# Kernel tuning notes

Measured on AMD Instinct MI355X. Metric: run time of the kernel, lower is better.

## Reference

```python
import jax, jax.numpy as jnp
import numpy as np

ANGLE_BINS = 16
RADIUS_BINS = 8


def _bilinear_cart(img, ys, xs):
    # img [B,C,H,W]; ys/xs: sample grid [A,R] in pixel coords, zero outside image
    h, w = img.shape[2], img.shape[3]
    y0 = jnp.floor(ys)
    x0 = jnp.floor(xs)
    wy = (ys - y0).astype(img.dtype)
    wx = (xs - x0).astype(img.dtype)
    y0i = jnp.clip(y0, 0, h - 1).astype(jnp.int32)
    y1i = jnp.clip(y0 + 1, 0, h - 1).astype(jnp.int32)
    x0i = jnp.clip(x0, 0, w - 1).astype(jnp.int32)
    x1i = jnp.clip(x0 + 1, 0, w - 1).astype(jnp.int32)
    v00 = img[:, :, y0i, x0i]
    v01 = img[:, :, y0i, x1i]
    v10 = img[:, :, y1i, x0i]
    v11 = img[:, :, y1i, x1i]
    out = (v00 * (1 - wy) * (1 - wx) + v01 * (1 - wy) * wx
           + v10 * wy * (1 - wx) + v11 * wy * wx)
    valid = ((ys >= 0) & (ys <= h - 1) & (xs >= 0) & (xs <= w - 1)).astype(img.dtype)
    return out * valid


def cartesian_to_polar(x):
    # [B,C,H,W] -> [B,C,ANGLE_BINS,RADIUS_BINS] via bilinear sampling on a polar grid
    b, c, h, w = x.shape
    cy = (h - 1) / 2.0
    cx = (w - 1) / 2.0
    max_r = min(h, w) / 2.0
    theta = 2.0 * jnp.pi * jnp.arange(ANGLE_BINS, dtype=jnp.float32) / ANGLE_BINS
    r = (jnp.arange(RADIUS_BINS, dtype=jnp.float32) + 0.5) / RADIUS_BINS * max_r
    ys = cy + r[None, :] * jnp.sin(theta)[:, None]  # [A,R]
    xs = cx + r[None, :] * jnp.cos(theta)[:, None]  # [A,R]
    return _bilinear_cart(x, ys, xs)


def polar_to_cartesian(pf, h, w):
    # [B,C,A,R] -> [B,C,H,W]: inverse remap with angular wrap, radial clamp,
    # zero outside the max radius disc
    b, c, A, R = pf.shape
    cy = (h - 1) / 2.0
    cx = (w - 1) / 2.0
    max_r = min(h, w) / 2.0
    yy, xx = jnp.meshgrid(jnp.arange(h, dtype=jnp.float32),
                          jnp.arange(w, dtype=jnp.float32), indexing='ij')
    dy = yy - cy
    dx = xx - cx
    rr = jnp.sqrt(dy * dy + dx * dx)
    th = jnp.mod(jnp.arctan2(dy, dx), 2.0 * jnp.pi)
    a = th / (2.0 * jnp.pi) * A
    ri = rr / max_r * R - 0.5
    a0 = jnp.floor(a)
    wa = (a - a0).astype(pf.dtype)
    a0i = jnp.mod(a0.astype(jnp.int32), A)
    a1i = jnp.mod(a0i + 1, A)
    r0 = jnp.floor(ri)
    wr = (ri - r0).astype(pf.dtype)
    r0i = jnp.clip(r0, 0, R - 1).astype(jnp.int32)
    r1i = jnp.clip(r0 + 1, 0, R - 1).astype(jnp.int32)
    v00 = pf[:, :, a0i, r0i]
    v01 = pf[:, :, a0i, r1i]
    v10 = pf[:, :, a1i, r0i]
    v11 = pf[:, :, a1i, r1i]
    out = (v00 * (1 - wa) * (1 - wr) + v01 * (1 - wa) * wr
           + v10 * wa * (1 - wr) + v11 * wa * wr)
    valid = (rr <= max_r).astype(pf.dtype)
    return out * valid


def setup_inputs() -> dict:
    key = jax.random.key(0)
    ks = jax.random.split(key, 4)
    B, C, H, W = 16, 256, 128, 128
    x = jax.random.normal(ks[0], (B, C, H, W), dtype=jnp.float32)
    # grouped 3x3 conv: groups=4 -> kernel [C_out=C, C_in/groups=C//4, 3, 3]
    w_polar = jax.random.normal(ks[1], (C, C // 4, 3, 3), dtype=jnp.float32) * 0.05
    b_polar = jnp.zeros((C,), jnp.float32)
    w_attn1 = jax.random.normal(ks[2], (C // 4, C), dtype=jnp.float32) * 0.05
    b_attn1 = jnp.zeros((C // 4,), jnp.float32)
    w_attn2 = jax.random.normal(ks[3], (1, C // 4), dtype=jnp.float32) * 0.05
    b_attn2 = jnp.zeros((1,), jnp.float32)
    return {"x": x, "w_polar": w_polar, "b_polar": b_polar,
            "w_attn1": w_attn1, "b_attn1": b_attn1,
            "w_attn2": w_attn2, "b_attn2": b_attn2}


def reference(x, w_polar, b_polar, w_attn1, b_attn1, w_attn2, b_attn2):
    b, c, h, w = x.shape
    pf = cartesian_to_polar(x)  # [B,C,16,8]
    pp = jax.lax.conv_general_dilated(
        pf, w_polar, window_strides=(1, 1), padding=((1, 1), (1, 1)),
        dimension_numbers=('NCHW', 'OIHW', 'NCHW'), feature_group_count=4)
    pp = pp + b_polar[None, :, None, None]
    pc = polar_to_cartesian(pp, h, w)  # [B,C,H,W]
    h1 = jax.nn.relu(jnp.einsum('bchw,oc->bohw', pc, w_attn1)
                     + b_attn1[None, :, None, None])
    att = jax.nn.sigmoid(jnp.einsum('bchw,oc->bohw', h1, w_attn2)
                         + b_attn2[None, :, None, None])  # [B,1,H,W]
    return x * att
```

## Files before the change

kernel.cpp:

```cpp
#include <hip/hip_runtime.h>
#include <math.h>

#define TWO_PI 6.28318530717958647692f

typedef float f4 __attribute__((ext_vector_type(4)));

__global__ __launch_bounds__(256) void k1_cart2polar(const float* __restrict__ x,
                                                     float* __restrict__ pf) {
    __shared__ float w00s[128], w01s[128], w10s[128], w11s[128];
    __shared__ int   o00s[128], o01s[128], o10s[128], o11s[128];
    int tid = threadIdx.x;
    if (tid < 128) {
        int a = tid >> 3, r = tid & 7;
        float theta = (TWO_PI * (float)a) / 16.0f;
        float rad   = ((float)r + 0.5f) / 8.0f * 64.0f;
        float ys = 63.5f + rad * sinf(theta);
        float xs = 63.5f + rad * cosf(theta);
        float y0 = floorf(ys), x0 = floorf(xs);
        float wy = ys - y0,    wx = xs - x0;
        int y0i = min(max((int)y0, 0), 127);
        int y1i = min(max((int)y0 + 1, 0), 127);
        int x0i = min(max((int)x0, 0), 127);
        int x1i = min(max((int)x0 + 1, 0), 127);
        float valid = (ys >= 0.0f && ys <= 127.0f && xs >= 0.0f && xs <= 127.0f) ? 1.0f : 0.0f;
        w00s[tid] = valid * (1.0f - wy) * (1.0f - wx);
        w01s[tid] = valid * (1.0f - wy) * wx;
        w10s[tid] = valid * wy * (1.0f - wx);
        w11s[tid] = valid * wy * wx;
        o00s[tid] = y0i * 128 + x0i;
        o01s[tid] = y0i * 128 + x1i;
        o10s[tid] = y1i * 128 + x0i;
        o11s[tid] = y1i * 128 + x1i;
    }
    __syncthreads();
    int t = blockIdx.x * 256 + tid;
    int bin = t & 127;
    int img = t >> 7;
    const float* ib = x + ((size_t)img << 14);
    float v = ib[o00s[bin]] * w00s[bin]
            + ib[o01s[bin]] * w01s[bin]
            + ib[o10s[bin]] * w10s[bin]
            + ib[o11s[bin]] * w11s[bin];
    pf[t] = v;
}

__global__ __launch_bounds__(128) void k2_conv(const float* __restrict__ pf,
                                               const float* __restrict__ w_polar,
                                               const float* __restrict__ b_polar,
                                               float* __restrict__ pp_t) {
    __shared__ __align__(16) float pfs[32 * 180];
    __shared__ __align__(16) float wls[32 * 72];
    int bid = blockIdx.x;
    int b  = bid >> 5;
    int g  = (bid >> 3) & 3;
    int ot = bid & 7;
    int tid = threadIdx.x;
    int a = tid >> 3, r = tid & 7;
    int oc0 = g * 64 + ot * 8;

    for (int i = tid; i < 32 * 180; i += 128) pfs[i] = 0.0f;
    __syncthreads();

    float acc[8];
    #pragma unroll
    for (int j = 0; j < 8; ++j) acc[j] = 0.0f;
    const float* src = pf + ((size_t)(b * 256 + g * 64) << 7);

    for (int pass = 0; pass < 2; ++pass) {
        for (int i = tid; i < 4096; i += 128) {
            int icl = i >> 7, bin = i & 127;
            pfs[icl * 180 + ((bin >> 3) + 1) * 10 + (bin & 7) + 1]
                = src[pass * 4096 + i];
        }
        for (int i = tid; i < 2304; i += 128) {
            int icl = i / 72, rem = i - icl * 72;
            int tap = rem >> 3, j = rem & 7;
            wls[i] = w_polar[(size_t)(oc0 + j) * 576 + (pass * 32 + icl) * 9 + tap];
        }
        __syncthreads();

        const float* pbase = pfs + a * 10 + r;
        for (int ic = 0; ic < 32; ++ic) {
            float v[9];
            const float* base = pbase + ic * 180;
            #pragma unroll
            for (int dh = 0; dh < 3; ++dh)
                #pragma unroll
                for (int dw = 0; dw < 3; ++dw)
                    v[dh * 3 + dw] = base[dh * 10 + dw];
            const f4* wrow = (const f4*)(wls + ic * 72);
            #pragma unroll
            for (int tap = 0; tap < 9; ++tap) {
                f4 wlo = wrow[tap * 2];
                f4 whi = wrow[tap * 2 + 1];
                float vt = v[tap];
                acc[0] += wlo.x * vt;  acc[1] += wlo.y * vt;
                acc[2] += wlo.z * vt;  acc[3] += wlo.w * vt;
                acc[4] += whi.x * vt;  acc[5] += whi.y * vt;
                acc[6] += whi.z * vt;  acc[7] += whi.w * vt;
            }
        }
        __syncthreads();
    }
    float* dst = pp_t + ((size_t)(b * 128 + tid)) * 256 + oc0;
    #pragma unroll
    for (int j = 0; j < 8; ++j) dst[j] = acc[j] + b_polar[oc0 + j];
}

__global__ __launch_bounds__(256) void k3_proj(const float* __restrict__ pp_t,
                                               const float* __restrict__ w_attn1,
                                               float* __restrict__ q) {
    __shared__ __align__(16) float wl[16384];
    int tid = threadIdx.x;
    for (int i = tid; i < 16384; i += 256) {
        int o = i >> 8, c = i & 255;
        wl[(c << 6) + (o ^ (c & 31))] = w_attn1[i];
    }
    __syncthreads();
    int n = blockIdx.x * 256 + tid;
    int b   = n >> 13;
    int bin = (n >> 6) & 127;
    int o   = n & 63;
    const float4* pr4 = (const float4*)(pp_t + ((size_t)((b << 7) + bin)) * 256);
    float acc = 0.0f;
    #pragma unroll 8
    for (int c4 = 0; c4 < 64; ++c4) {
        float4 p = pr4[c4];
        int c = c4 << 2;
        acc += wl[( c      << 6) + (o ^ ( c      & 31))] * p.x;
        acc += wl[((c + 1) << 6) + (o ^ ((c + 1) & 31))] * p.y;
        acc += wl[((c + 2) << 6) + (o ^ ((c + 2) & 31))] * p.z;
        acc += wl[((c + 3) << 6) + (o ^ ((c + 3) & 31))] * p.w;
    }
    q[n] = acc;
}

__global__ __launch_bounds__(256) void k4a_att(const float* __restrict__ q,
                                               const float* __restrict__ b_attn1,
                                               const float* __restrict__ w_attn2,
                                               const float* __restrict__ b_attn2,
                                               float* __restrict__ att) {
    __shared__ __align__(16) float qs[8896];
    __shared__ __align__(16) float b1s[64];
    __shared__ __align__(16) float w2s[64];
    int b    = blockIdx.x >> 6;
    int tile = blockIdx.x & 63;
    int tid  = threadIdx.x;
    const float* qb = q + ((size_t)b << 13);
    for (int i = tid; i < 8192; i += 256) {
        int bin = i >> 6, o = i & 63;
        qs[(bin >> 3) * 556 + (bin & 7) * 68 + o] = qb[i];
    }
    if (tid < 64) { b1s[tid] = b_attn1[tid]; w2s[tid] = w_attn2[tid]; }
    __syncthreads();
    float b2 = b_attn2[0];
    const float4* q4  = (const float4*)qs;
    const float4* b14 = (const float4*)b1s;
    const float4* w24 = (const float4*)w2s;

    int p = (tile << 8) + tid;
    int h = p >> 7, w = p & 127;
    float dy = (float)h - 63.5f;
    float dx = (float)w - 63.5f;
    float rr = sqrtf(dy * dy + dx * dx);
    float th = atan2f(dy, dx);
    if (th < 0.0f) th += TWO_PI;
    float aa = th / TWO_PI * 16.0f;
    float a0 = floorf(aa);
    float wa = aa - a0;
    int ia0 = ((int)a0) & 15;
    int ia1 = (ia0 + 1) & 15;
    float ri = rr / 64.0f * 8.0f - 0.5f;
    float r0 = floorf(ri);
    float wr = ri - r0;
    int ir0 = (int)fminf(fmaxf(r0, 0.0f), 7.0f);
    int ir1 = (int)fminf(fmaxf(r0 + 1.0f, 0.0f), 7.0f);
    float valid = (rr <= 64.0f) ? 1.0f : 0.0f;
    float w00 = valid * (1.0f - wa) * (1.0f - wr);
    float w01 = valid * (1.0f - wa) * wr;
    float w10 = valid * wa * (1.0f - wr);
    float w11 = valid * wa * wr;
    int t00 = ia0 * 139 + ir0 * 17;
    int t01 = ia0 * 139 + ir1 * 17;
    int t10 = ia1 * 139 + ir0 * 17;
    int t11 = ia1 * 139 + ir1 * 17;
    float acc = b2;
    #pragma unroll
    for (int i = 0; i < 16; ++i) {
        float4 v00 = q4[t00 + i], v01 = q4[t01 + i];
        float4 v10 = q4[t10 + i], v11 = q4[t11 + i];
        float4 bb = b14[i], ww = w24[i];
        float sx = w00 * v00.x + w01 * v01.x + w10 * v10.x + w11 * v11.x;
        float sy = w00 * v00.y + w01 * v01.y + w10 * v10.y + w11 * v11.y;
        float sz = w00 * v00.z + w01 * v01.z + w10 * v10.z + w11 * v11.z;
        float sw = w00 * v00.w + w01 * v01.w + w10 * v10.w + w11 * v11.w;
        acc += fmaxf(sx + bb.x, 0.0f) * ww.x;
        acc += fmaxf(sy + bb.y, 0.0f) * ww.y;
        acc += fmaxf(sz + bb.z, 0.0f) * ww.z;
        acc += fmaxf(sw + bb.w, 0.0f) * ww.w;
    }
    float attv = 1.0f / (1.0f + __expf(-acc));
    att[((size_t)b << 14) + p] = attv;
}

__global__ __launch_bounds__(256) void k4b_mul(const f4* __restrict__ x4,
                                               const float* __restrict__ att,
                                               f4* __restrict__ out4) {
    const f4* att4 = (const f4*)att;
    int idx = blockIdx.x * 256 + threadIdx.x;
    int stride = gridDim.x * 256;
    for (int i = idx; i < 16777216; i += stride) {
        f4 xv = __builtin_nontemporal_load(&x4[i]);
        f4 av = att4[((i >> 20) << 12) | (i & 4095)];
        __builtin_nontemporal_store(xv * av, &out4[i]);
    }
}

extern "C" void kernel_launch(void* const* d_in, const int* in_sizes, int n_in,
                              void* d_out, int out_size, void* d_ws, size_t ws_size,
                              hipStream_t stream) {
    const float* x       = (const float*)d_in[0];
    const float* w_polar = (const float*)d_in[1];
    const float* b_polar = (const float*)d_in[2];
    const float* w_attn1 = (const float*)d_in[3];
    const float* b_attn1 = (const float*)d_in[4];
    const float* w_attn2 = (const float*)d_in[5];
    const float* b_attn2 = (const float*)d_in[6];
    float* out = (float*)d_out;
    float* ws  = (float*)d_ws;

    float* pf   = ws;
    float* pp_t = ws + 524288;
    float* q    = ws + 1048576;
    float* att  = ws + 1179648;

    hipLaunchKernelGGL(k1_cart2polar, dim3(2048), dim3(256), 0, stream, x, pf);
    hipLaunchKernelGGL(k2_conv,       dim3(512),  dim3(128), 0, stream,
                       pf, w_polar, b_polar, pp_t);
    hipLaunchKernelGGL(k3_proj,       dim3(512),  dim3(256), 0, stream, pp_t, w_attn1, q);
    hipLaunchKernelGGL(k4a_att,       dim3(1024), dim3(256), 0, stream,
                       q, b_attn1, w_attn2, b_attn2, att);
    hipLaunchKernelGGL(k4b_mul,       dim3(2048), dim3(256), 0, stream,
                       (const f4*)x, att, (f4*)out);
}
```

Measured before the change: 160.6 us.

## Restructure grouped polar conv into register-blocked tiles with all group channels per block

The grouped 3x3 polar convolution now has each block handle all 64 output channels of a group for half the angle rows. Each thread computes 4 output channels for 4 adjacent radius bins, reusing a 3x6 input window across radius positions. Weights are staged in shared memory transposed so each tap gives a float4 over output channels, and outputs are written as float4 stores. This cuts redundant input staging across the eight output tiles and raises arithmetic per shared load, but the grid drops from 512 to 128 blocks, which may underfill the GPU.

Result: slower. 171.4 us (+6.7%).

```diff
diff --git a/kernel.cpp b/kernel.cpp
--- a/kernel.cpp
+++ b/kernel.cpp
@@ -44,67 +44,70 @@
     pf[t] = v;
 }
 
-__global__ __launch_bounds__(128) void k2_conv(const float* __restrict__ pf,
+__global__ __launch_bounds__(256) void k2_conv(const float* __restrict__ pf,
                                                const float* __restrict__ w_polar,
                                                const float* __restrict__ b_polar,
                                                float* __restrict__ pp_t) {
-    __shared__ __align__(16) float pfs[32 * 180];
-    __shared__ __align__(16) float wls[32 * 72];
+    __shared__ __align__(16) float pfs[16 * 180];
+    __shared__ __align__(16) float wls[16 * 612];
     int bid = blockIdx.x;
-    int b  = bid >> 5;
-    int g  = (bid >> 3) & 3;
-    int ot = bid & 7;
+    int b    = bid >> 3;
+    int g    = (bid >> 1) & 3;
+    int half = bid & 1;
     int tid = threadIdx.x;
-    int a = tid >> 3, r = tid & 7;
-    int oc0 = g * 64 + ot * 8;
-
-    for (int i = tid; i < 32 * 180; i += 128) pfs[i] = 0.0f;
-    __syncthreads();
-
-    float acc[8];
-    #pragma unroll
-    for (int j = 0; j < 8; ++j) acc[j] = 0.0f;
-    const float* src = pf + ((size_t)(b * 256 + g * 64) << 7);
-
-    for (int pass = 0; pass < 2; ++pass) {
-        for (int i = tid; i < 4096; i += 128) {
+    int bg     = tid >> 4;
+    int ocslot = tid & 15;
+    int a  = (half << 3) | (bg >> 1);
+    int R0 = (bg & 1) << 2;
+
+    f4 acc4[4] = {};
+    const float* src  = pf + ((size_t)(b * 256 + g * 64)) * 128;
+    const float* wsrc = w_polar + (size_t)g * 64 * 576;
+
+    for (int i = tid; i < 16 * 180; i += 256) pfs[i] = 0.0f;
+
+    for (int pass = 0; pass < 4; ++pass) {
+        __syncthreads();
+        for (int i = tid; i < 2048; i += 256) {
             int icl = i >> 7, bin = i & 127;
             pfs[icl * 180 + ((bin >> 3) + 1) * 10 + (bin & 7) + 1]
-                = src[pass * 4096 + i];
+                = src[(pass * 16 + icl) * 128 + bin];
         }
-        for (int i = tid; i < 2304; i += 128) {
-            int icl = i / 72, rem = i - icl * 72;
-            int tap = rem >> 3, j = rem & 7;
-            wls[i] = w_polar[(size_t)(oc0 + j) * 576 + (pass * 32 + icl) * 9 + tap];
+        for (int i = tid; i < 9216; i += 256) {
+            int ocr = i / 144, rem = i - ocr * 144;
+            int icl = rem / 9,  tap = rem - icl * 9;
+            wls[icl * 612 + tap * 68 + ocr] = wsrc[ocr * 576 + pass * 144 + rem];
         }
         __syncthreads();
 
-        const float* pbase = pfs + a * 10 + r;
-        for (int ic = 0; ic < 32; ++ic) {
-            float v[9];
-            const float* base = pbase + ic * 180;
+        for (int ic = 0; ic < 16; ++ic) {
+            float v[3][6];
+            const float* pb = pfs + ic * 180 + a * 10 + R0;
             #pragma unroll
             for (int dh = 0; dh < 3; ++dh)
                 #pragma unroll
-                for (int dw = 0; dw < 3; ++dw)
-                    v[dh * 3 + dw] = base[dh * 10 + dw];
-            const f4* wrow = (const f4*)(wls + ic * 72);
+                for (int k = 0; k < 6; ++k)
+                    v[dh][k] = pb[dh * 10 + k];
+            const float* wb = wls + ic * 612 + ocslot * 4;
             #pragma unroll
-            for (int tap = 0; tap < 9; ++tap) {
-                f4 wlo = wrow[tap * 2];
-                f4 whi = wrow[tap * 2 + 1];
-                float vt = v[tap];
-                acc[0] += wlo.x * vt;  acc[1] += wlo.y * vt;
-                acc[2] += wlo.z * vt;  acc[3] += wlo.w * vt;
-                acc[4] += whi.x * vt;  acc[5] += whi.y * vt;
-                acc[6] += whi.z * vt;  acc[7] += whi.w * vt;
-            }
+            for (int dh = 0; dh < 3; ++dh)
+                #pragma unroll
+                for (int dw = 0; dw < 3; ++dw) {
+                    f4 wv = *(const f4*)(wb + (dh * 3 + dw) * 68);
+                    #pragma unroll
+                    for (int rb = 0; rb < 4; ++rb)
+                        acc4[rb] += wv * v[dh][dw + rb];
+                }
         }
-        __syncthreads();
-    }
-    float* dst = pp_t + ((size_t)(b * 128 + tid)) * 256 + oc0;
+    }
+
+    f4 bias = *(const f4*)(b_polar + g * 64 + ocslot * 4);
     #pragma unroll
-    for (int j = 0; j < 8; ++j) dst[j] = acc[j] + b_polar[oc0 + j];
+    for (int rb = 0; rb < 4; ++rb) {
+        int bi = a * 8 + R0 + rb;
+        *(f4*)(pp_t + ((size_t)(b * 128 + bi)) * 256 + g * 64 + ocslot * 4)
+            = acc4[rb] + bias;
+    }
 }
 
 __global__ __launch_bounds__(256) void k3_proj(const float* __restrict__ pp_t,
@@ -235,7 +238,7 @@
     float* att  = ws + 1179648;
 
     hipLaunchKernelGGL(k1_cart2polar, dim3(2048), dim3(256), 0, stream, x, pf);
-    hipLaunchKernelGGL(k2_conv,       dim3(512),  dim3(128), 0, stream,
+    hipLaunchKernelGGL(k2_conv,       dim3(128),  dim3(256), 0, stream,
                        pf, w_polar, b_polar, pp_t);
     hipLaunchKernelGGL(k3_proj,       dim3(512),  dim3(256), 0, stream, pp_t, w_attn1, q);
     hipLaunchKernelGGL(k4a_att,       dim3(1024), dim3(256), 0, stream,
```
